# Kernel tuning notes

Measured on AMD Instinct MI355X. Metric: run time of the kernel, lower is better.

Reference implementation:

```python
import jax, jax.numpy as jnp
import numpy as np

B, S, D = 4, 2048, 1024  # batch, seq_len, d_model == d_internal


def setup_inputs() -> dict:
    key = jax.random.key(0)
    ks = jax.random.split(key, 7)
    s = 1.0 / np.sqrt(D)  # scale weights so softmax / relu stay in a sane range
    return {
        "input_vecs": jax.random.normal(ks[0], (B, S, D), jnp.float32),
        "Wq": jax.random.normal(ks[1], (D, D), jnp.float32) * s,
        "Wk": jax.random.normal(ks[2], (D, D), jnp.float32) * s,
        "Wv": jax.random.normal(ks[3], (D, D), jnp.float32) * s,
        "W1": jax.random.normal(ks[4], (D, D), jnp.float32) * s,  # linear1: d_internal -> d_model
        "b1": jnp.zeros((D,), jnp.float32),
        "W2": jax.random.normal(ks[5], (D, D), jnp.float32) * s,  # linear2: d_model -> d_internal
        "b2": jnp.zeros((D,), jnp.float32),
    }


def reference(input_vecs, Wq, Wk, Wv, W1, b1, W2, b2):
    d_internal = Wq.shape[1]
    # single-head self-attention: Q,K,V = X @ Wq/Wk/Wv
    q = jnp.einsum("bsd,de->bse", input_vecs, Wq)
    k = jnp.einsum("bsd,de->bse", input_vecs, Wk)
    v = jnp.einsum("bsd,de->bse", input_vecs, Wv)
    scores = jnp.einsum("bqe,bke->bqk", q, k) / jnp.sqrt(jnp.asarray(d_internal, q.dtype))
    attn = jax.nn.softmax(scores, axis=-1)               # [B, S, S]
    attn_out = jnp.einsum("bqk,bke->bqe", attn, v)       # [B, S, D]
    h = attn_out + input_vecs                            # residual 1
    h = jax.nn.relu(h @ W1 + b1)                         # linear1 + relu
    out = h @ W2 + b2 + input_vecs                       # linear2 + residual 2
    return out, attn
```

## Files before the change

kernel.cpp:

```cpp
#include <hip/hip_runtime.h>
#include <hip/hip_bf16.h>

typedef unsigned short u16;
typedef unsigned int   u32;
typedef u16   u16x8 __attribute__((ext_vector_type(8)));
typedef u16   u16x4 __attribute__((ext_vector_type(4)));
typedef __bf16 bf16x8 __attribute__((ext_vector_type(8)));
typedef float f32x4 __attribute__((ext_vector_type(4)));

__device__ __forceinline__ u16 f2bf(float f) {
    u32 u = __float_as_uint(f);
    u = u + 0x7FFFu + ((u >> 16) & 1u);
    return (u16)(u >> 16);
}

__device__ __forceinline__ void gload16(const u16* g, u16* l) {
    __builtin_amdgcn_global_load_lds(
        (const __attribute__((address_space(1))) void*)g,
        (__attribute__((address_space(3))) void*)l,
        16, 0, 0);
}

#define WAITV(N) asm volatile("s_waitcnt vmcnt(" #N ")" ::: "memory")
#define SCHEDB() __builtin_amdgcn_sched_barrier(0)
#define BAR()    __builtin_amdgcn_s_barrier()

__global__ __launch_bounds__(256) void cvt_x(const float* __restrict__ X,
                                             u16* __restrict__ Xb) {
    const long i = (long)(blockIdx.x * 256 + threadIdx.x) * 8;
    float4 a = *(const float4*)(X + i);
    float4 b = *(const float4*)(X + i + 4);
    u16x8 r;
    r[0] = f2bf(a.x); r[1] = f2bf(a.y); r[2] = f2bf(a.z); r[3] = f2bf(a.w);
    r[4] = f2bf(b.x); r[5] = f2bf(b.y); r[6] = f2bf(b.z); r[7] = f2bf(b.w);
    *(u16x8*)(Xb + i) = r;
}

__global__ __launch_bounds__(256) void cvt_wT(const float* __restrict__ w0,
                                              const float* __restrict__ w1,
                                              const float* __restrict__ w2,
                                              const float* __restrict__ w3,
                                              const float* __restrict__ w4,
                                              u16* __restrict__ wt) {
    const float* srcs[5] = {w0, w1, w2, w3, w4};
    const float* W = srcs[blockIdx.z];
    u16* WT = wt + (long)blockIdx.z * 1048576;
    __shared__ float t[32][33];
    const int tx = threadIdx.x, ty = threadIdx.y;
    const int n0 = blockIdx.x * 32, k0 = blockIdx.y * 32;
    #pragma unroll
    for (int r = 0; r < 4; ++r)
        t[ty + 8 * r][tx] = W[(long)(k0 + ty + 8 * r) * 1024 + n0 + tx];
    __syncthreads();
    #pragma unroll
    for (int r = 0; r < 4; ++r)
        WT[(long)(n0 + ty + 8 * r) * 1024 + k0 + tx] = f2bf(t[tx][ty + 8 * r]);
}

#define BM 256
#define BN 128
#define BKW 64
#define SLOT_A (BM * BKW)
#define SLOT_B (BN * BKW)
#define SLOTSZ (SLOT_A + SLOT_B)

enum { EPI_QKV = 0, EPI_SCALE_F32 = 2, EPI_ADDX_BF16 = 3,
       EPI_BIAS_RELU_BF16 = 4, EPI_BIAS_ADDX_F32 = 5 };

template <int EPI>
__global__ __launch_bounds__(512, 1)
void gemm_bt(const u16* __restrict__ A, const u16* __restrict__ Bt,
             void* __restrict__ Cout, void* __restrict__ CoutK,
             void* __restrict__ CoutV,
             const float* __restrict__ bias, const float* __restrict__ Xres,
             const int M, const int N, const int K,
             const long sA, const long sB, const long sC, const long sX,
             const float scale) {
    const int GX = gridDim.x, GY = gridDim.y;
    const int p  = blockIdx.x + GX * (blockIdx.y + GY * blockIdx.z);
    const int slab = (p & 7) + 8 * (p / (8 * GY));
    const int vy   = (p >> 3) % GY;
    const int vx   = slab % GX;
    const int vz   = slab / GX;

    const int bz = vz;
    const u16* Ab = A + (long)bz * sA;
    const u16* Bb = Bt + (long)bz * sB;
    const float* Xr = Xres ? Xres + (long)bz * sX : nullptr;

    const int tid  = threadIdx.x;
    const int lane = tid & 63;
    const int w    = tid >> 6;
    const int wrg  = (w >> 1) * 64;
    const int wcg  = (w & 1) * 64;
    const int m0   = vx * BM;
    const int n0   = vy * BN;

    __shared__ __align__(16) u16 LDS[3 * SLOTSZ];

    f32x4 acc[4][4] = {};

    const long Kl = K;
    const int schunk = ((lane & 7) ^ (lane >> 3)) * 8;
    const u16* Ag = Ab + (long)(m0 + w * 32 + (lane >> 3)) * Kl + schunk;
    const u16* Bg = Bb + (long)(n0 + w * 16 + (lane >> 3)) * Kl + schunk;

    const int rbase = lane & 15;
    const int rx    = rbase & 7;
    const int q4    = lane >> 4;

    const int dAoff = (w * 32) * BKW;
    const int dBoff = SLOT_A + (w * 16) * BKW;

    #define LDA(mi, ks) (*(const bf16x8*)(Asl + (wrg + (mi) * 16 + rbase) * BKW \
                         + ((((ks) * 4 + q4) ^ rx)) * 8))
    #define LDB(ni, ks) (*(const bf16x8*)(Bsl + (wcg + (ni) * 16 + rbase) * BKW \
                         + ((((ks) * 4 + q4) ^ rx)) * 8))

    const int nt = K / BKW;
    {
        u16* d0 = &LDS[0];
        gload16(Ag, d0 + dAoff);
        gload16(Ag + 8 * Kl,  d0 + dAoff + 512);
        gload16(Ag + 16 * Kl, d0 + dAoff + 1024);
        gload16(Ag + 24 * Kl, d0 + dAoff + 1536);
        gload16(Bg, d0 + dBoff);
        gload16(Bg + 8 * Kl,  d0 + dBoff + 512);
        u16* d1 = &LDS[SLOTSZ];
        gload16(Ag + BKW, d1 + dAoff);
        gload16(Ag + BKW + 8 * Kl,  d1 + dAoff + 512);
        gload16(Ag + BKW + 16 * Kl, d1 + dAoff + 1024);
        gload16(Ag + BKW + 24 * Kl, d1 + dAoff + 1536);
        gload16(Bg + BKW, d1 + dBoff);
        gload16(Bg + BKW + 8 * Kl,  d1 + dBoff + 512);
    }
    WAITV(6);
    BAR();

    int s = 0;
    for (int t = 0; t < nt; ++t) {
        const u16* Asl = &LDS[s * SLOTSZ];
        const u16* Bsl = &LDS[s * SLOTSZ + SLOT_A];
        const int s2 = (s + 2 >= 3) ? s - 1 : s + 2;
        u16* dA = &LDS[s2 * SLOTSZ] + dAoff;
        u16* dB = &LDS[s2 * SLOTSZ] + dBoff;
        const bool st = (t + 2 < nt);
        const long kt2 = (long)(t + 2) * BKW;

        bf16x8 af[4], bf[4];

        if (st) {
            gload16(Ag + kt2, dA);
            gload16(Ag + kt2 + 8 * Kl, dA + 512);
            gload16(Bg + kt2, dB);
        }
        #pragma unroll
        for (int mi = 0; mi < 4; ++mi) af[mi] = LDA(mi, 0);
        #pragma unroll
        for (int ni = 0; ni < 4; ++ni) bf[ni] = LDB(ni, 0);
        SCHEDB(); BAR();
        __builtin_amdgcn_s_setprio(1);
        #pragma unroll
        for (int mi = 0; mi < 4; ++mi)
            #pragma unroll
            for (int ni = 0; ni < 4; ++ni)
                acc[mi][ni] = __builtin_amdgcn_mfma_f32_16x16x32_bf16(
                    af[mi], bf[ni], acc[mi][ni], 0, 0, 0);
        __builtin_amdgcn_s_setprio(0);
        SCHEDB(); BAR();

        if (st) {
            gload16(Ag + kt2 + 16 * Kl, dA + 1024);
            gload16(Ag + kt2 + 24 * Kl, dA + 1536);
            gload16(Bg + kt2 + 8 * Kl, dB + 512);
        }
        #pragma unroll
        for (int mi = 0; mi < 4; ++mi) af[mi] = LDA(mi, 1);
        #pragma unroll
        for (int ni = 0; ni < 4; ++ni) bf[ni] = LDB(ni, 1);
        SCHEDB(); BAR();
        __builtin_amdgcn_s_setprio(1);
        #pragma unroll
        for (int mi = 0; mi < 4; ++mi)
            #pragma unroll
            for (int ni = 0; ni < 4; ++ni)
                acc[mi][ni] = __builtin_amdgcn_mfma_f32_16x16x32_bf16(
                    af[mi], bf[ni], acc[mi][ni], 0, 0, 0);
        __builtin_amdgcn_s_setprio(0);
        SCHEDB();
        if (st) { WAITV(6); } else { WAITV(0); }
        BAR();

        s = (s == 2) ? 0 : s + 1;
    }
    #undef LDA
    #undef LDB

    const int colb = wcg + (lane & 15);
    const int rq   = (lane >> 4) * 4;
    #pragma unroll
    for (int mi = 0; mi < 4; ++mi) {
        #pragma unroll
        for (int ni = 0; ni < 4; ++ni) {
            f32x4 v = acc[mi][ni];
            const int gr0 = m0 + wrg + mi * 16 + rq;
            const int gc  = n0 + colb + ni * 16;
            if constexpr (EPI == EPI_QKV) {
                if (bz == 2) {
                    u16x4 p2;
                    p2[0] = f2bf(v[0]); p2[1] = f2bf(v[1]);
                    p2[2] = f2bf(v[2]); p2[3] = f2bf(v[3]);
                    u16* C = (u16*)CoutV;
                    const long off = ((long)(gr0 >> 11)) * 2097152 +
                                     (long)gc * 2048 + (gr0 & 2047);
                    *(u16x4*)(C + off) = p2;
                } else {
                    u16* C = (u16*)(bz == 0 ? Cout : CoutK);
                    #pragma unroll
                    for (int j = 0; j < 4; ++j)
                        C[(long)(gr0 + j) * N + gc] = f2bf(v[j]);
                }
            } else {
                #pragma unroll
                for (int j = 0; j < 4; ++j) {
                    const long idx = (long)(gr0 + j) * N + gc;
                    float val = v[j];
                    if constexpr (EPI == EPI_SCALE_F32) {
                        ((float*)Cout + (long)bz * sC)[idx] = val * scale;
                    } else if constexpr (EPI == EPI_ADDX_BF16) {
                        val += Xr[idx];
                        ((u16*)Cout + (long)bz * sC)[idx] = f2bf(val);
                    } else if constexpr (EPI == EPI_BIAS_RELU_BF16) {
                        val = fmaxf(val + bias[gc], 0.0f);
                        ((u16*)Cout + (long)bz * sC)[idx] = f2bf(val);
                    } else if constexpr (EPI == EPI_BIAS_ADDX_F32) {
                        ((float*)Cout + (long)bz * sC)[idx] =
                            val + bias[gc] + Xr[idx];
                    }
                }
            }
        }
    }
}

__global__ __launch_bounds__(256)
void softmax_rows(float* __restrict__ attn, u16* __restrict__ P) {
    const int row  = blockIdx.x;
    float* rp      = attn + (long)row * 2048;
    const int tid  = threadIdx.x;
    const int lane = tid & 63;
    const int w    = tid >> 6;

    float4 v0 = *(const float4*)(rp + tid * 8);
    float4 v1 = *(const float4*)(rp + tid * 8 + 4);

    float m = fmaxf(fmaxf(fmaxf(v0.x, v0.y), fmaxf(v0.z, v0.w)),
                    fmaxf(fmaxf(v1.x, v1.y), fmaxf(v1.z, v1.w)));
    #pragma unroll
    for (int o = 32; o > 0; o >>= 1) m = fmaxf(m, __shfl_xor(m, o));
    __shared__ float redm[4];
    if (lane == 0) redm[w] = m;
    __syncthreads();
    m = fmaxf(fmaxf(redm[0], redm[1]), fmaxf(redm[2], redm[3]));

    float e[8];
    e[0] = __expf(v0.x - m); e[1] = __expf(v0.y - m);
    e[2] = __expf(v0.z - m); e[3] = __expf(v0.w - m);
    e[4] = __expf(v1.x - m); e[5] = __expf(v1.y - m);
    e[6] = __expf(v1.z - m); e[7] = __expf(v1.w - m);
    float s = ((e[0] + e[1]) + (e[2] + e[3])) + ((e[4] + e[5]) + (e[6] + e[7]));
    #pragma unroll
    for (int o = 32; o > 0; o >>= 1) s += __shfl_xor(s, o);
    __shared__ float reds[4];
    if (lane == 0) reds[w] = s;
    __syncthreads();
    s = (reds[0] + reds[1]) + (reds[2] + reds[3]);
    const float inv = 1.0f / s;

    float4 o0, o1;
    o0.x = e[0] * inv; o0.y = e[1] * inv; o0.z = e[2] * inv; o0.w = e[3] * inv;
    o1.x = e[4] * inv; o1.y = e[5] * inv; o1.z = e[6] * inv; o1.w = e[7] * inv;
    *(float4*)(rp + tid * 8)     = o0;
    *(float4*)(rp + tid * 8 + 4) = o1;

    u16x8 pb;
    pb[0] = f2bf(o0.x); pb[1] = f2bf(o0.y); pb[2] = f2bf(o0.z); pb[3] = f2bf(o0.w);
    pb[4] = f2bf(o1.x); pb[5] = f2bf(o1.y); pb[6] = f2bf(o1.z); pb[7] = f2bf(o1.w);
    *(u16x8*)(P + (long)row * 2048 + tid * 8) = pb;
}

extern "C" void kernel_launch(void* const* d_in, const int* in_sizes, int n_in,
                              void* d_out, int out_size, void* d_ws, size_t ws_size,
                              hipStream_t stream) {
    const float* X  = (const float*)d_in[0];
    const float* Wq = (const float*)d_in[1];
    const float* Wk = (const float*)d_in[2];
    const float* Wv = (const float*)d_in[3];
    const float* W1 = (const float*)d_in[4];
    const float* b1 = (const float*)d_in[5];
    const float* W2 = (const float*)d_in[6];
    const float* b2 = (const float*)d_in[7];

    float* out  = (float*)d_out;
    float* attn = out + (size_t)8388608;

    char* ws = (char*)d_ws;
    u16* Xb  = (u16*)(ws);
    u16* Qb  = (u16*)(ws + (size_t)16 * 1024 * 1024);
    u16* Kb  = (u16*)(ws + (size_t)32 * 1024 * 1024);
    u16* VT  = (u16*)(ws + (size_t)48 * 1024 * 1024);
    u16* H1b = (u16*)(ws + (size_t)64 * 1024 * 1024);
    u16* WTs = (u16*)(ws + (size_t)80 * 1024 * 1024);
    u16* W1T = WTs + (size_t)3 * 1048576;
    u16* W2T = WTs + (size_t)4 * 1048576;
    u16* Pb  = Xb;
    u16* Hb  = Kb;

    cvt_x<<<4096, 256, 0, stream>>>(X, Xb);
    cvt_wT<<<dim3(32, 32, 5), dim3(32, 8), 0, stream>>>(Wq, Wk, Wv, W1, W2, WTs);

    gemm_bt<EPI_QKV><<<dim3(32, 8, 3), 512, 0, stream>>>(
        Xb, WTs, Qb, Kb, VT, nullptr, nullptr, 8192, 1024, 1024,
        0, 1048576, 0, 0, 1.0f);

    gemm_bt<EPI_SCALE_F32><<<dim3(8, 16, 4), 512, 0, stream>>>(
        Qb, Kb, attn, nullptr, nullptr, nullptr, nullptr, 2048, 2048, 1024,
        2048L * 1024, 2048L * 1024, 2048L * 2048, 0, 0.03125f);

    softmax_rows<<<8192, 256, 0, stream>>>(attn, Pb);

    gemm_bt<EPI_ADDX_BF16><<<dim3(8, 8, 4), 512, 0, stream>>>(
        Pb, VT, Hb, nullptr, nullptr, nullptr, X, 2048, 1024, 2048,
        2048L * 2048, 1024L * 2048, 2048L * 1024, 2048L * 1024, 1.0f);

    gemm_bt<EPI_BIAS_RELU_BF16><<<dim3(32, 8, 1), 512, 0, stream>>>(
        Hb, W1T, H1b, nullptr, nullptr, b1, nullptr, 8192, 1024, 1024,
        0, 0, 0, 0, 1.0f);

    gemm_bt<EPI_BIAS_ADDX_F32><<<dim3(32, 8, 1), 512, 0, stream>>>(
        H1b, W2T, out, nullptr, nullptr, b2, X, 8192, 1024, 1024,
        0, 0, 0, 0, 1.0f);
}
```

Baseline: 253.1 us.

## Add 256x256-tile double-buffered GEMM kernel for QKV and QK^T projections

Adds a new gemm_big kernel with 256x256 output tiles, a two-stage LDS double buffer, staggered A/B global-to-LDS staging, and MFMA phases raised with s_setprio. It is used for the QKV projection and the QK^T score GEMM, replacing the 256x128 triple-buffered kernel. The larger tile raises arithmetic intensity and halves the block count. In exchange each wave holds 128 accumulator floats, the launch bound now asks for two blocks per CU, and the extra barriers may limit overlap. The older kernel drops its unused QKV and scale epilogues and the extra output pointers.

```diff
diff --git a/kernel.cpp b/kernel.cpp
--- a/kernel.cpp
+++ b/kernel.cpp
@@ -57,6 +57,189 @@
         WT[(long)(n0 + ty + 8 * r) * 1024 + k0 + tx] = f2bf(t[tx][ty + 8 * r]);
 }
 
+enum { EPI_QKV = 0, EPI_SCALE_F32 = 2, EPI_ADDX_BF16 = 3,
+       EPI_BIAS_RELU_BF16 = 4, EPI_BIAS_ADDX_F32 = 5 };
+
+#define GBM 256
+#define GBN 256
+#define GBK 64
+#define GSLOT_A (GBM * GBK)
+#define GSLOTSZ (2 * GSLOT_A)
+
+template <int EPI>
+__global__ __launch_bounds__(512, 2)
+void gemm_big(const u16* __restrict__ A, const u16* __restrict__ Bt,
+              void* __restrict__ Cout, void* __restrict__ CoutK,
+              void* __restrict__ CoutV,
+              const int N, const int K,
+              const long sA, const long sB, const long sC,
+              const float scale) {
+    const int GX = gridDim.x, GY = gridDim.y;
+    const int p  = blockIdx.x + GX * (blockIdx.y + GY * blockIdx.z);
+    const int slab = (p & 7) + 8 * (p / (8 * GY));
+    const int vy   = (p >> 3) % GY;
+    const int vx   = slab % GX;
+    const int bz   = slab / GX;
+
+    const u16* Ab = A + (long)bz * sA;
+    const u16* Bb = Bt + (long)bz * sB;
+
+    const int tid  = threadIdx.x;
+    const int lane = tid & 63;
+    const int w    = tid >> 6;
+    const int wrg  = (w >> 2) * 128;
+    const int wcg  = (w & 3) * 64;
+    const int m0   = vx * GBM;
+    const int n0   = vy * GBN;
+
+    __shared__ __align__(16) u16 LDS[2 * GSLOTSZ];
+
+    f32x4 acc[8][4] = {};
+
+    const long Kl = K;
+    const int schunk = ((lane & 7) ^ (lane >> 3)) * 8;
+    const u16* Ag = Ab + (long)(m0 + w * 32 + (lane >> 3)) * Kl + schunk;
+    const u16* Bg = Bb + (long)(n0 + w * 32 + (lane >> 3)) * Kl + schunk;
+
+    const int rbase = lane & 15;
+    const int rx    = rbase & 7;
+    const int q4    = lane >> 4;
+
+    const int dAoff = (w * 32) * GBK;
+    const int dBoff = GSLOT_A + (w * 32) * GBK;
+
+    #define GLDA(mi, ks) (*(const bf16x8*)(Asl + (wrg + (mi) * 16 + rbase) * GBK \
+                          + ((((ks) * 4 + q4) ^ rx)) * 8))
+    #define GLDB(ni, ks) (*(const bf16x8*)(Bsl + (wcg + (ni) * 16 + rbase) * GBK \
+                          + ((((ks) * 4 + q4) ^ rx)) * 8))
+    #define GSTAGE_A(KT, D) do {                       \
+        gload16(Ag + (KT), (D));                       \
+        gload16(Ag + (KT) + 8 * Kl,  (D) + 512);       \
+        gload16(Ag + (KT) + 16 * Kl, (D) + 1024);      \
+        gload16(Ag + (KT) + 24 * Kl, (D) + 1536);      \
+    } while (0)
+    #define GSTAGE_B(KT, D) do {                       \
+        gload16(Bg + (KT), (D));                       \
+        gload16(Bg + (KT) + 8 * Kl,  (D) + 512);       \
+        gload16(Bg + (KT) + 16 * Kl, (D) + 1024);      \
+        gload16(Bg + (KT) + 24 * Kl, (D) + 1536);      \
+    } while (0)
+    #define GMFMA2(mi)                                                         \
+        _Pragma("unroll")                                                      \
+        for (int ni = 0; ni < 4; ++ni) {                                       \
+            acc[mi][ni] = __builtin_amdgcn_mfma_f32_16x16x32_bf16(             \
+                af0, bf[ni][0], acc[mi][ni], 0, 0, 0);                         \
+            acc[mi][ni] = __builtin_amdgcn_mfma_f32_16x16x32_bf16(             \
+                af1, bf[ni][1], acc[mi][ni], 0, 0, 0);                         \
+        }
+
+    const int nt = K / GBK;
+    GSTAGE_A(0, &LDS[0] + dAoff);
+    GSTAGE_B(0, &LDS[0] + dBoff);
+    WAITV(0);
+    BAR();
+
+    for (int t = 0; t < nt; ++t) {
+        const int s = t & 1;
+        const u16* Asl = &LDS[s * GSLOTSZ];
+        const u16* Bsl = &LDS[s * GSLOTSZ] + GSLOT_A;
+        u16* dnx = &LDS[(s ^ 1) * GSLOTSZ];
+        const bool st = (t + 1 < nt);
+        const long kt1 = (long)(t + 1) * GBK;
+
+        bf16x8 bf[4][2], af0, af1;
+
+        if (st) GSTAGE_A(kt1, dnx + dAoff);
+        SCHEDB();
+        #pragma unroll
+        for (int ni = 0; ni < 4; ++ni) {
+            bf[ni][0] = GLDB(ni, 0);
+            bf[ni][1] = GLDB(ni, 1);
+        }
+        { af0 = GLDA(0, 0); af1 = GLDA(0, 1); }
+        bf16x8 an0 = GLDA(1, 0), an1 = GLDA(1, 1);
+        SCHEDB(); BAR();
+        __builtin_amdgcn_s_setprio(1);
+        GMFMA2(0);
+        { af0 = an0; af1 = an1; }
+        GMFMA2(1);
+        __builtin_amdgcn_s_setprio(0);
+        SCHEDB(); BAR();
+
+        if (st) GSTAGE_B(kt1, dnx + dBoff);
+        SCHEDB();
+        { af0 = GLDA(2, 0); af1 = GLDA(2, 1); }
+        an0 = GLDA(3, 0); an1 = GLDA(3, 1);
+        SCHEDB(); BAR();
+        __builtin_amdgcn_s_setprio(1);
+        GMFMA2(2);
+        { af0 = an0; af1 = an1; }
+        GMFMA2(3);
+        __builtin_amdgcn_s_setprio(0);
+        SCHEDB(); BAR();
+
+        { af0 = GLDA(4, 0); af1 = GLDA(4, 1); }
+        an0 = GLDA(5, 0); an1 = GLDA(5, 1);
+        SCHEDB(); BAR();
+        __builtin_amdgcn_s_setprio(1);
+        GMFMA2(4);
+        { af0 = an0; af1 = an1; }
+        GMFMA2(5);
+        __builtin_amdgcn_s_setprio(0);
+        SCHEDB(); BAR();
+
+        { af0 = GLDA(6, 0); af1 = GLDA(6, 1); }
+        an0 = GLDA(7, 0); an1 = GLDA(7, 1);
+        SCHEDB(); BAR();
+        __builtin_amdgcn_s_setprio(1);
+        GMFMA2(6);
+        { af0 = an0; af1 = an1; }
+        GMFMA2(7);
+        __builtin_amdgcn_s_setprio(0);
+        SCHEDB();
+        WAITV(0);
+        BAR();
+    }
+    #undef GLDA
+    #undef GLDB
+    #undef GSTAGE_A
+    #undef GSTAGE_B
+    #undef GMFMA2
+
+    const int colb = wcg + (lane & 15);
+    const int rq   = (lane >> 4) * 4;
+    #pragma unroll
+    for (int mi = 0; mi < 8; ++mi) {
+        #pragma unroll
+        for (int ni = 0; ni < 4; ++ni) {
+            f32x4 v = acc[mi][ni];
+            const int gr0 = m0 + wrg + mi * 16 + rq;
+            const int gc  = n0 + colb + ni * 16;
+            if constexpr (EPI == EPI_QKV) {
+                if (bz == 2) {
+                    u16x4 p2;
+                    p2[0] = f2bf(v[0]); p2[1] = f2bf(v[1]);
+                    p2[2] = f2bf(v[2]); p2[3] = f2bf(v[3]);
+                    u16* C = (u16*)CoutV;
+                    const long off = ((long)(gr0 >> 11)) * 2097152 +
+                                     (long)gc * 2048 + (gr0 & 2047);
+                    *(u16x4*)(C + off) = p2;
+                } else {
+                    u16* C = (u16*)(bz == 0 ? Cout : CoutK);
+                    #pragma unroll
+                    for (int j = 0; j < 4; ++j)
+                        C[(long)(gr0 + j) * N + gc] = f2bf(v[j]);
+                }
+            } else if constexpr (EPI == EPI_SCALE_F32) {
+                float* C = (float*)Cout + (long)bz * sC;
+                #pragma unroll
+                for (int j = 0; j < 4; ++j)
+                    C[(long)(gr0 + j) * N + gc] = v[j] * scale;
+            }
+        }
+    }
+}
+
 #define BM 256
 #define BN 128
 #define BKW 64
@@ -64,14 +247,10 @@
 #define SLOT_B (BN * BKW)
 #define SLOTSZ (SLOT_A + SLOT_B)
 
-enum { EPI_QKV = 0, EPI_SCALE_F32 = 2, EPI_ADDX_BF16 = 3,
-       EPI_BIAS_RELU_BF16 = 4, EPI_BIAS_ADDX_F32 = 5 };
-
 template <int EPI>
 __global__ __launch_bounds__(512, 1)
 void gemm_bt(const u16* __restrict__ A, const u16* __restrict__ Bt,
-             void* __restrict__ Cout, void* __restrict__ CoutK,
-             void* __restrict__ CoutV,
+             void* __restrict__ Cout,
              const float* __restrict__ bias, const float* __restrict__ Xres,
              const int M, const int N, const int K,
              const long sA, const long sB, const long sC, const long sX,
@@ -205,38 +384,19 @@
             f32x4 v = acc[mi][ni];
             const int gr0 = m0 + wrg + mi * 16 + rq;
             const int gc  = n0 + colb + ni * 16;
-            if constexpr (EPI == EPI_QKV) {
-                if (bz == 2) {
-                    u16x4 p2;
-                    p2[0] = f2bf(v[0]); p2[1] = f2bf(v[1]);
-                    p2[2] = f2bf(v[2]); p2[3] = f2bf(v[3]);
-                    u16* C = (u16*)CoutV;
-                    const long off = ((long)(gr0 >> 11)) * 2097152 +
-                                     (long)gc * 2048 + (gr0 & 2047);
-                    *(u16x4*)(C + off) = p2;
-                } else {
-                    u16* C = (u16*)(bz == 0 ? Cout : CoutK);
-                    #pragma unroll
-                    for (int j = 0; j < 4; ++j)
-                        C[(long)(gr0 + j) * N + gc] = f2bf(v[j]);
-                }
-            } else {
-                #pragma unroll
-                for (int j = 0; j < 4; ++j) {
-                    const long idx = (long)(gr0 + j) * N + gc;
-                    float val = v[j];
-                    if constexpr (EPI == EPI_SCALE_F32) {
-                        ((float*)Cout + (long)bz * sC)[idx] = val * scale;
-                    } else if constexpr (EPI == EPI_ADDX_BF16) {
-                        val += Xr[idx];
-                        ((u16*)Cout + (long)bz * sC)[idx] = f2bf(val);
-                    } else if constexpr (EPI == EPI_BIAS_RELU_BF16) {
-                        val = fmaxf(val + bias[gc], 0.0f);
-                        ((u16*)Cout + (long)bz * sC)[idx] = f2bf(val);
-                    } else if constexpr (EPI == EPI_BIAS_ADDX_F32) {
-                        ((float*)Cout + (long)bz * sC)[idx] =
-                            val + bias[gc] + Xr[idx];
-                    }
+            #pragma unroll
+            for (int j = 0; j < 4; ++j) {
+                const long idx = (long)(gr0 + j) * N + gc;
+                float val = v[j];
+                if constexpr (EPI == EPI_ADDX_BF16) {
+                    val += Xr[idx];
+                    ((u16*)Cout + (long)bz * sC)[idx] = f2bf(val);
+                } else if constexpr (EPI == EPI_BIAS_RELU_BF16) {
+                    val = fmaxf(val + bias[gc], 0.0f);
+                    ((u16*)Cout + (long)bz * sC)[idx] = f2bf(val);
+                } else if constexpr (EPI == EPI_BIAS_ADDX_F32) {
+                    ((float*)Cout + (long)bz * sC)[idx] =
+                        val + bias[gc] + Xr[idx];
                 }
             }
         }
@@ -319,25 +479,22 @@
     cvt_x<<<4096, 256, 0, stream>>>(X, Xb);
     cvt_wT<<<dim3(32, 32, 5), dim3(32, 8), 0, stream>>>(Wq, Wk, Wv, W1, W2, WTs);
 
-    gemm_bt<EPI_QKV><<<dim3(32, 8, 3), 512, 0, stream>>>(
-        Xb, WTs, Qb, Kb, VT, nullptr, nullptr, 8192, 1024, 1024,
-        0, 1048576, 0, 0, 1.0f);
-
-    gemm_bt<EPI_SCALE_F32><<<dim3(8, 16, 4), 512, 0, stream>>>(
-        Qb, Kb, attn, nullptr, nullptr, nullptr, nullptr, 2048, 2048, 1024,
-        2048L * 1024, 2048L * 1024, 2048L * 2048, 0, 0.03125f);
+    gemm_big<EPI_QKV><<<dim3(32, 4, 3), 512, 0, stream>>>(
+        Xb, WTs, Qb, Kb, VT, 1024, 1024, 0, 1048576, 0, 1.0f);
+
+    gemm_big<EPI_SCALE_F32><<<dim3(8, 8, 4), 512, 0, stream>>>(
+        Qb, Kb, attn, nullptr, nullptr, 2048, 1024,
+        2048L * 1024, 2048L * 1024, 2048L * 2048, 0.03125f);
 
     softmax_rows<<<8192, 256, 0, stream>>>(attn, Pb);
 
     gemm_bt<EPI_ADDX_BF16><<<dim3(8, 8, 4), 512, 0, stream>>>(
-        Pb, VT, Hb, nullptr, nullptr, nullptr, X, 2048, 1024, 2048,
+        Pb, VT, Hb, nullptr, X, 2048, 1024, 2048,
         2048L * 2048, 1024L * 2048, 2048L * 1024, 2048L * 1024, 1.0f);
 
     gemm_bt<EPI_BIAS_RELU_BF16><<<dim3(32, 8, 1), 512, 0, stream>>>(
-        Hb, W1T, H1b, nullptr, nullptr, b1, nullptr, 8192, 1024, 1024,
-        0, 0, 0, 0, 1.0f);
+        Hb, W1T, H1b, b1, nullptr, 8192, 1024, 1024, 0, 0, 0, 0, 1.0f);
 
     gemm_bt<EPI_BIAS_ADDX_F32><<<dim3(32, 8, 1), 512, 0, stream>>>(
-        H1b, W2T, out, nullptr, nullptr, b2, X, 8192, 1024, 1024,
-        0, 0, 0, 0, 1.0f);
-}
+        H1b, W2T, out, b2, X, 8192, 1024, 1024, 0, 0, 0, 0, 1.0f);
+}
```

Measured after the change: 249.3 us. No clear change (-1.5%).
